# Kernel optimization log

Hardware: AMD Instinct MI355X
Metric: run time of the kernel (lower is better)

The kernel has to match this reference:

```python
import jax, jax.numpy as jnp
import numpy as np

EMBED_DIM = 2048
N_HEAD = 16
N_KV_HEAD = 4
HEAD_DIM = EMBED_DIM // N_HEAD  # 128
GROUP = N_HEAD // N_KV_HEAD     # 4
SCALE = HEAD_DIM ** -0.5
B, T = 2, 2048


def setup_inputs() -> dict:
    key = jax.random.key(0)
    ks = jax.random.split(key, 5)
    s = 0.02
    # weights stored as [in, out] (y = x @ W); equivalent to torch Linear W.T
    return {
        "x": jax.random.normal(ks[0], (B, T, EMBED_DIM), jnp.float32),
        "Wq": jax.random.normal(ks[1], (EMBED_DIM, EMBED_DIM), jnp.float32) * s,
        "Wk": jax.random.normal(ks[2], (EMBED_DIM, N_KV_HEAD * HEAD_DIM), jnp.float32) * s,
        "Wv": jax.random.normal(ks[3], (EMBED_DIM, N_KV_HEAD * HEAD_DIM), jnp.float32) * s,
        "Wo": jax.random.normal(ks[4], (EMBED_DIM, EMBED_DIM), jnp.float32) * s,
    }


def reference(x, Wq, Wk, Wv, Wo):
    # Prefill path (T>1, no cache): GQA causal attention, eval mode (dropout=0).
    Bq, Tq, C = x.shape
    q = (x @ Wq).reshape(Bq, Tq, N_HEAD, HEAD_DIM).transpose(0, 2, 1, 3)      # (B,Hq,T,D)
    k = (x @ Wk).reshape(Bq, Tq, N_KV_HEAD, HEAD_DIM).transpose(0, 2, 1, 3)  # (B,Hkv,T,D)
    v = (x @ Wv).reshape(Bq, Tq, N_KV_HEAD, HEAD_DIM).transpose(0, 2, 1, 3)
    # expand_kv: each kv head repeated GROUP times consecutively
    k = jnp.repeat(k, GROUP, axis=1)  # (B,Hq,T,D)
    v = jnp.repeat(v, GROUP, axis=1)
    scores = jnp.einsum("bhqd,bhkd->bhqk", q, k) * SCALE
    causal = jnp.tril(jnp.ones((Tq, Tq), dtype=bool))
    scores = jnp.where(causal[None, None], scores, jnp.finfo(scores.dtype).min)
    probs = jax.nn.softmax(scores, axis=-1)
    atten = jnp.einsum("bhqk,bhkd->bhqd", probs, v)
    atten = atten.transpose(0, 2, 1, 3).reshape(Bq, Tq, C)
    out = atten @ Wo
    return out
```

## Files before the change

### kernel.cpp

```cpp
#include <hip/hip_runtime.h>

typedef unsigned short u16;
typedef unsigned int   u32;
typedef __attribute__((ext_vector_type(4))) float  f32x4;
typedef __attribute__((ext_vector_type(8))) __bf16 bf16x8;

#define EMBED 2048
#define NH    16
#define NKV   4
#define HD    128
#define TT    2048
#define BB    2
#define MROWS (BB*TT)
#define QSCALE 0.08838834764831845f

#define QELEMS ((size_t)BB*NH*TT*HD)
#define KELEMS ((size_t)BB*NKV*TT*HD)

#define AS1(p) (__attribute__((address_space(1))) void*)(void*)(p)
#define AS3(p) (__attribute__((address_space(3))) void*)(void*)(p)


static __device__ __forceinline__ u16 f2b(float f){
  union { float f; u32 u; } v; v.f = f;
  u32 u = v.u;
  u32 r = u + 0x7FFFu + ((u >> 16) & 1u);
  return (u16)(r >> 16);
}

__global__ __launch_bounds__(256) void cvt_f32_bf16(const float* __restrict__ in,
                                                    u16* __restrict__ out, int n4){
  int i = blockIdx.x * 256 + threadIdx.x;
  if (i >= n4) return;
  float4 v = ((const float4*)in)[i];
  uint2 o;
  o.x = (u32)f2b(v.x) | ((u32)f2b(v.y) << 16);
  o.y = (u32)f2b(v.z) | ((u32)f2b(v.w) << 16);
  ((uint2*)out)[i] = o;
}

__global__ __launch_bounds__(256) void trans_w2(const float* __restrict__ in0, u16* __restrict__ out0,
                                                const float* __restrict__ in1, u16* __restrict__ out1,
                                                int R, int C){
  const float* in = blockIdx.z ? in1 : in0;
  u16*        out = blockIdx.z ? out1 : out0;
  __shared__ u16 tile[32][33];
  int c0 = blockIdx.x * 32, r0 = blockIdx.y * 32;
  int tx = threadIdx.x & 31, ty = threadIdx.x >> 5;
  #pragma unroll
  for (int j = 0; j < 32; j += 8)
    tile[ty + j][tx] = f2b(in[(size_t)(r0 + ty + j) * C + c0 + tx]);
  __syncthreads();
  #pragma unroll
  for (int j = 0; j < 32; j += 8)
    out[(size_t)(c0 + ty + j) * R + r0 + tx] = tile[tx][ty + j];
}

__global__ __launch_bounds__(256) void trans_v(const u16* __restrict__ in,
                                               u16* __restrict__ out){
  __shared__ u16 tile[32][33];
  int d0 = (blockIdx.x & 3) * 32;
  int t0 = ((blockIdx.x >> 2) & 63) * 32;
  int bh = blockIdx.x >> 8;
  const u16* ip = in  + (size_t)bh * TT * HD;
  u16*       op = out + (size_t)bh * TT * HD;
  int tx = threadIdx.x & 31, ty = threadIdx.x >> 5;
  #pragma unroll
  for (int j = 0; j < 32; j += 8)
    tile[ty + j][tx] = ip[(size_t)(t0 + ty + j) * HD + d0 + tx];
  __syncthreads();
  #pragma unroll
  for (int j = 0; j < 32; j += 8)
    op[(size_t)(d0 + ty + j) * TT + t0 + tx] = tile[tx][ty + j];
}

template<int EPI>
__global__ __launch_bounds__(256)
void gemm_bt(const u16* __restrict__ A, const u16* __restrict__ Bt,
             void* __restrict__ outp, int N, int K){
  __shared__ __align__(16) u16 As[2][128*32];
  __shared__ __align__(16) u16 Bs[2][128*32];
  int tid  = threadIdx.x;
  int lane = tid & 63, w = tid >> 6;
  int nwg = gridDim.x;
  int bid = blockIdx.x;
  bid = (bid & 7) * (nwg >> 3) + (bid >> 3);
  int nbn  = N >> 7;
  int brow = (bid / nbn) * 128;
  int bcol = (bid % nbn) * 128;

  auto stage = [&](int buf, int kt){
    #pragma unroll
    for (int j = 0; j < 2; ++j){
      int boff  = w * 2048 + j * 1024;
      int chunk = (boff >> 4) + lane;
      int row   = chunk >> 2;
      int cko   = chunk & 3;
      const u16* ga = A  + (size_t)(brow + row) * K + kt + cko * 8;
      const u16* gb = Bt + (size_t)(bcol + row) * K + kt + cko * 8;
      __builtin_amdgcn_global_load_lds(AS1(ga), AS3(&As[buf][boff >> 1]), 16, 0, 0);
      __builtin_amdgcn_global_load_lds(AS1(gb), AS3(&Bs[buf][boff >> 1]), 16, 0, 0);
    }
  };

  int lr = lane & 15, lg = lane >> 4, lk = lg * 8;
  int wr = (w >> 1) * 64, wc = (w & 1) * 64;

  f32x4 acc[4][4];
  #pragma unroll
  for (int m = 0; m < 4; ++m)
    #pragma unroll
    for (int n = 0; n < 4; ++n)
      #pragma unroll
      for (int r = 0; r < 4; ++r) acc[m][n][r] = 0.f;

  int NT = K >> 5;
  stage(0, 0);
  asm volatile("s_waitcnt vmcnt(0)" ::: "memory");
  __syncthreads();
  int cur = 0;
  for (int t = 0; t < NT; ++t){
    if (t + 1 < NT) stage(cur ^ 1, (t + 1) * 32);
    const u16* as = As[cur];
    const u16* bs = Bs[cur];
    bf16x8 af[4], bfv[4];
    #pragma unroll
    for (int m = 0; m < 4; ++m) af[m]  = *(const bf16x8*)(as + (wr + m*16 + lr)*32 + lk);
    #pragma unroll
    for (int n = 0; n < 4; ++n) bfv[n] = *(const bf16x8*)(bs + (wc + n*16 + lr)*32 + lk);
    #pragma unroll
    for (int m = 0; m < 4; ++m)
      #pragma unroll
      for (int n = 0; n < 4; ++n)
        acc[m][n] = __builtin_amdgcn_mfma_f32_16x16x32_bf16(af[m], bfv[n], acc[m][n], 0, 0, 0);
    asm volatile("s_waitcnt vmcnt(0)" ::: "memory");
    __syncthreads();
    cur ^= 1;
  }

  if (EPI == 0){
    float* o = (float*)outp;
    #pragma unroll
    for (int m = 0; m < 4; ++m)
      #pragma unroll
      for (int r = 0; r < 4; ++r){
        int rowg = brow + wr + m*16 + lg*4 + r;
        float* orow = o + (size_t)rowg * N + bcol + wc + lr;
        #pragma unroll
        for (int n = 0; n < 4; ++n) orow[n*16] = acc[m][n][r];
      }
  } else {
    u16* qb = (u16*)outp;
    u16* kb = qb + QELEMS;
    u16* vb = kb + KELEMS;
    int hb = bcol >> 7;
    int b  = brow >> 11;
    u16* hp; float s;
    if (hb < 16)      { hp = qb + ((size_t)(b*NH  +  hb     )) * TT * HD; s = QSCALE; }
    else if (hb < 20) { hp = kb + ((size_t)(b*NKV + (hb-16))) * TT * HD; s = 1.0f; }
    else              { hp = vb + ((size_t)(b*NKV + (hb-20))) * TT * HD; s = 1.0f; }
    #pragma unroll
    for (int m = 0; m < 4; ++m)
      #pragma unroll
      for (int r = 0; r < 4; ++r){
        int t = (brow + wr + m*16 + lg*4 + r) & (TT - 1);
        #pragma unroll
        for (int n = 0; n < 4; ++n){
          int d = wc + n*16 + lr;
          hp[(size_t)t * HD + d] = f2b(acc[m][n][r] * s);
        }
      }
  }
}

__global__ __launch_bounds__(256)
void attn_kernel(const u16* __restrict__ qb, const u16* __restrict__ kb,
                 const u16* __restrict__ vtb, u16* __restrict__ ob){
  __shared__ __align__(16) u16 Ks[2][64*128];
  __shared__ __align__(16) u16 Vs[2][128*64];
  int tid = threadIdx.x, lane = tid & 63, w = tid >> 6;
  int nwg = gridDim.x;
  int bid = blockIdx.x;
  bid = (bid & 7) * (nwg >> 3) + (bid >> 3);
  int pair = bid & 15;
  int h    = (bid >> 4) & 15;
  int b    = bid >> 8;
  int hkv  = h >> 2;
  int j  = lane & 15, g = lane >> 4, lk = g * 8;
  int gh = g >> 1;
  int sw = (j & 7) << 3;

  const u16* qbase = qb  + ((size_t)b * NH  + h  ) * TT * HD;
  const u16* kbase = kb  + ((size_t)b * NKV + hkv) * TT * HD;
  const u16* vbase = vtb + ((size_t)b * NKV + hkv) * HD * TT;

  auto stage = [&](int buf, int kt){
    #pragma unroll
    for (int i = 0; i < 4; ++i){
      int c  = i * 256 + tid;
      int ub = (i * 256 + w * 64) * 8;
      int kr = c >> 4, kc = (c & 15) ^ (kr & 7);
      const u16* gk = kbase + (size_t)(kt * 64 + kr) * HD + kc * 8;
      __builtin_amdgcn_global_load_lds(AS1(gk), AS3(&Ks[buf][ub]), 16, 0, 0);
      int vr = c >> 3, vc = (c & 7) ^ (vr & 7);
      const u16* gv = vbase + (size_t)vr * TT + kt * 64 + vc * 8;
      __builtin_amdgcn_global_load_lds(AS1(gv), AS3(&Vs[buf][ub]), 16, 0, 0);
    }
  };

  for (int half = 0; half < 2; ++half){
    int qt = half ? (31 - pair) : pair;
    int q0 = qt * 64 + w * 16;

    bf16x8 aq[4];
    #pragma unroll
    for (int s = 0; s < 4; ++s)
      aq[s] = *(const bf16x8*)(qbase + (size_t)(q0 + j) * HD + s*32 + lk);

    f32x4 o_acc[8];
    #pragma unroll
    for (int dt = 0; dt < 8; ++dt)
      #pragma unroll
      for (int r = 0; r < 4; ++r) o_acc[dt][r] = 0.f;
    float mrow = -1e30f, lrow = 0.f;

    __builtin_amdgcn_s_barrier();
    stage(0, 0);
    int cur = 0;
    for (int kt = 0; kt <= qt; ++kt){
      __builtin_amdgcn_s_barrier();
      if (kt < qt){
        stage(cur ^ 1, kt + 1);
        asm volatile("s_waitcnt vmcnt(8)" ::: "memory");
      } else {
        asm volatile("s_waitcnt vmcnt(0)" ::: "memory");
      }
      __builtin_amdgcn_s_barrier();

      const u16* ks = Ks[cur];
      f32x4 sc[4];
      #pragma unroll
      for (int c = 0; c < 4; ++c)
        #pragma unroll
        for (int r = 0; r < 4; ++r) sc[c][r] = 0.f;
      __builtin_amdgcn_s_setprio(1);
      #pragma unroll
      for (int c = 0; c < 4; ++c){
        const u16* kp = ks + (c*16 + j) * 128;
        #pragma unroll
        for (int s = 0; s < 4; ++s){
          bf16x8 kf = *(const bf16x8*)(kp + (((s*32) + lk) ^ sw));
          sc[c] = __builtin_amdgcn_mfma_f32_16x16x32_bf16(kf, aq[s], sc[c], 0, 0, 0);
        }
      }
      __builtin_amdgcn_s_setprio(0);
      if (kt == qt){
        int qg = q0 + j;
        #pragma unroll
        for (int c = 0; c < 4; ++c)
          #pragma unroll
          for (int r = 0; r < 4; ++r)
            if (kt*64 + c*16 + g*4 + r > qg) sc[c][r] = -1e30f;
      }
      float tm = fmaxf(fmaxf(fmaxf(sc[0][0], sc[0][1]), fmaxf(sc[0][2], sc[0][3])),
                       fmaxf(fmaxf(sc[1][0], sc[1][1]), fmaxf(sc[1][2], sc[1][3])));
      tm = fmaxf(tm, fmaxf(fmaxf(fmaxf(sc[2][0], sc[2][1]), fmaxf(sc[2][2], sc[2][3])),
                           fmaxf(fmaxf(sc[3][0], sc[3][1]), fmaxf(sc[3][2], sc[3][3]))));
      tm = fmaxf(tm, __shfl_xor(tm, 16));
      tm = fmaxf(tm, __shfl_xor(tm, 32));
      if (__any((tm > mrow + 8.f) ? 1 : 0)){
        float mnew  = fmaxf(mrow, tm);
        float alpha = __expf(mrow - mnew);
        mrow = mnew;
        lrow *= alpha;
        #pragma unroll
        for (int r = 0; r < 4; ++r){
          float ar = __shfl(alpha, (lane & 48) | (g*4 + r));
          #pragma unroll
          for (int dt = 0; dt < 8; ++dt) o_acc[dt][r] *= ar;
        }
      }
      float rs = 0.f;
      #pragma unroll
      for (int c = 0; c < 4; ++c)
        #pragma unroll
        for (int r = 0; r < 4; ++r){
          float p = __expf(sc[c][r] - mrow);
          sc[c][r] = p;
          rs += p;
        }
      rs += __shfl_xor(rs, 16);
      rs += __shfl_xor(rs, 32);
      lrow += rs;
      u32 pk[4][2];
      #pragma unroll
      for (int c = 0; c < 4; ++c){
        asm("v_cvt_pk_bf16_f32 %0, %1, %2" : "=v"(pk[c][0]) : "v"(sc[c][0]), "v"(sc[c][1]));
        asm("v_cvt_pk_bf16_f32 %0, %1, %2" : "=v"(pk[c][1]) : "v"(sc[c][2]), "v"(sc[c][3]));
      }
      bf16x8 pa[2];
      #pragma unroll
      for (int kk = 0; kk < 2; ++kk){
        u32 a0 = pk[2*kk + gh][0],       a1 = pk[2*kk + gh][1];
        u32 b0 = pk[2*kk + (gh ^ 1)][0], b1 = pk[2*kk + (gh ^ 1)][1];
        u32 v16_0 = (u32)__shfl_xor((int)a0, 16), v16_1 = (u32)__shfl_xor((int)a1, 16);
        u32 v32_0 = (u32)__shfl_xor((int)b0, 32), v32_1 = (u32)__shfl_xor((int)b1, 32);
        u32 v48_0 = (u32)__shfl_xor((int)b0, 48), v48_1 = (u32)__shfl_xor((int)b1, 48);
        union { u32 uw[4]; bf16x8 v; } u;
        u.uw[0] = (g==0) ? pk[2*kk][0]   : (g==1) ? v48_0 : (g==2) ? v32_0 : v16_0;
        u.uw[1] = (g==0) ? pk[2*kk][1]   : (g==1) ? v48_1 : (g==2) ? v32_1 : v16_1;
        u.uw[2] = (g==0) ? v16_0 : (g==1) ? v32_0 : (g==2) ? v48_0 : pk[2*kk+1][0];
        u.uw[3] = (g==0) ? v16_1 : (g==1) ? v32_1 : (g==2) ? v48_1 : pk[2*kk+1][1];
        pa[kk] = u.v;
      }
      const u16* vs = Vs[cur];
      __builtin_amdgcn_s_setprio(1);
      #pragma unroll
      for (int dt = 0; dt < 8; ++dt){
        const u16* vp = vs + (dt*16 + j) * 64;
        #pragma unroll
        for (int kk = 0; kk < 2; ++kk){
          bf16x8 vf = *(const bf16x8*)(vp + (((kk*32) + lk) ^ sw));
          o_acc[dt] = __builtin_amdgcn_mfma_f32_16x16x32_bf16(pa[kk], vf, o_acc[dt], 0, 0, 0);
        }
      }
      __builtin_amdgcn_s_setprio(0);
      cur ^= 1;
    }
    #pragma unroll
    for (int r = 0; r < 4; ++r){
      float ls  = __shfl(lrow, (lane & 48) | (g*4 + r));
      float inv = 1.0f / ls;
      int t = q0 + g*4 + r;
      size_t base = ((size_t)b * TT + t) * EMBED + h * HD;
      #pragma unroll
      for (int dt = 0; dt < 8; ++dt)
        ob[base + dt*16 + j] = f2b(o_acc[dt][r] * inv);
    }
  }
}

extern "C" void kernel_launch(void* const* d_in, const int* in_sizes, int n_in,
                              void* d_out, int out_size, void* d_ws, size_t ws_size,
                              hipStream_t stream){
  const float* x  = (const float*)d_in[0];
  const float* Wq = (const float*)d_in[1];
  const float* Wk = (const float*)d_in[2];
  const float* Wv = (const float*)d_in[3];
  const float* Wo = (const float*)d_in[4];

  char* ws = (char*)d_ws;
  size_t off = 0;
  auto alloc = [&](size_t bytes){ void* p = ws + off; off += (bytes + 255) & ~(size_t)255; return p; };
  u16* xb    = (u16*)alloc((size_t)MROWS * EMBED * 2);
  u16* Wqkvt = (u16*)alloc((size_t)3072 * EMBED * 2);
  u16* Wot   = (u16*)alloc((size_t)EMBED * EMBED * 2);
  u16* qkv   = (u16*)alloc((QELEMS + 2*KELEMS) * 2);
  u16* vtb   = (u16*)alloc(KELEMS * 2);
  u16* ob    = (u16*)alloc((size_t)MROWS * EMBED * 2);

  u16* qb = qkv;
  u16* kb = qb + QELEMS;
  u16* vb = kb + KELEMS;

  cvt_f32_bf16<<<(MROWS*EMBED/4 + 255)/256, 256, 0, stream>>>(x, xb, MROWS*EMBED/4);
  trans_w2<<<dim3(EMBED/32, EMBED/32, 2), 256, 0, stream>>>(Wq, Wqkvt, Wo, Wot, EMBED, EMBED);
  trans_w2<<<dim3(512/32,   EMBED/32, 2), 256, 0, stream>>>(Wk, Wqkvt + (size_t)2048*EMBED,
                                                            Wv, Wqkvt + (size_t)2560*EMBED, EMBED, 512);

  gemm_bt<2><<<(MROWS/128)*(3072/128), 256, 0, stream>>>(xb, Wqkvt, qkv, 3072, EMBED);
  trans_v<<<4*64*BB*NKV, 256, 0, stream>>>(vb, vtb);

  attn_kernel<<<BB*NH*16, 256, 0, stream>>>(qb, kb, vtb, ob);

  gemm_bt<0><<<(MROWS/128)*(EMBED/128), 256, 0, stream>>>(ob, Wot, d_out, EMBED, EMBED);
}
```

Baseline: 313.3 us.

## Use 128-row query tiles with two 16-row subtiles per wave in attention

The attention kernel now gives each workgroup a 128-row query tile, and each wave handles 32 query rows as two 16-row subtiles sharing every K/V fragment read from LDS. This halves the K/V staging traffic per query row and doubles the MFMA work per LDS read. The paired causal-balancing scheme (pair / 31-pair) is replaced by a longest-first ordering across 512 blocks, and launch bounds request two workgroups per SIMD. In exchange, register pressure roughly doubles (two sets of accumulators and Q fragments), which may force spills or lower occupancy, and the per-block causal work is now unbalanced.

```diff
diff --git a/kernel.cpp b/kernel.cpp
--- a/kernel.cpp
+++ b/kernel.cpp
@@ -173,19 +173,20 @@
   }
 }
 
-__global__ __launch_bounds__(256)
+__global__ __launch_bounds__(256, 2)
 void attn_kernel(const u16* __restrict__ qb, const u16* __restrict__ kb,
                  const u16* __restrict__ vtb, u16* __restrict__ ob){
   __shared__ __align__(16) u16 Ks[2][64*128];
   __shared__ __align__(16) u16 Vs[2][128*64];
   int tid = threadIdx.x, lane = tid & 63, w = tid >> 6;
-  int nwg = gridDim.x;
   int bid = blockIdx.x;
-  bid = (bid & 7) * (nwg >> 3) + (bid >> 3);
-  int pair = bid & 15;
-  int h    = (bid >> 4) & 15;
-  int b    = bid >> 8;
-  int hkv  = h >> 2;
+  int decoded = (bid & 7) * 64 + (bid >> 3);
+  int grp = decoded >> 6;
+  int i   = decoded & 63;
+  int qt  = 15 - (i & 15);
+  int h   = (grp & 3) * 4 + (i >> 4);
+  int b   = grp >> 2;
+  int hkv = h >> 2;
   int j  = lane & 15, g = lane >> 4, lk = g * 8;
   int gh = g >> 1;
   int sw = (j & 7) << 3;
@@ -196,9 +197,9 @@
 
   auto stage = [&](int buf, int kt){
     #pragma unroll
-    for (int i = 0; i < 4; ++i){
-      int c  = i * 256 + tid;
-      int ub = (i * 256 + w * 64) * 8;
+    for (int ii = 0; ii < 4; ++ii){
+      int c  = ii * 256 + tid;
+      int ub = (ii * 256 + w * 64) * 8;
       int kr = c >> 4, kc = (c & 15) ^ (kr & 7);
       const u16* gk = kbase + (size_t)(kt * 64 + kr) * HD + kc * 8;
       __builtin_amdgcn_global_load_lds(AS1(gk), AS3(&Ks[buf][ub]), 16, 0, 0);
@@ -208,76 +209,80 @@
     }
   };
 
-  for (int half = 0; half < 2; ++half){
-    int qt = half ? (31 - pair) : pair;
-    int q0 = qt * 64 + w * 16;
-
-    bf16x8 aq[4];
-    #pragma unroll
-    for (int s = 0; s < 4; ++s)
-      aq[s] = *(const bf16x8*)(qbase + (size_t)(q0 + j) * HD + s*32 + lk);
-
-    f32x4 o_acc[8];
-    #pragma unroll
-    for (int dt = 0; dt < 8; ++dt)
-      #pragma unroll
-      for (int r = 0; r < 4; ++r) o_acc[dt][r] = 0.f;
-    float mrow = -1e30f, lrow = 0.f;
-
+  int q0w = qt * 128 + w * 32;
+
+  bf16x8 aqA[4], aqB[4];
+  #pragma unroll
+  for (int s = 0; s < 4; ++s){
+    aqA[s] = *(const bf16x8*)(qbase + (size_t)(q0w + j)      * HD + s*32 + lk);
+    aqB[s] = *(const bf16x8*)(qbase + (size_t)(q0w + 16 + j) * HD + s*32 + lk);
+  }
+
+  f32x4 oA[8], oB[8];
+  #pragma unroll
+  for (int dt = 0; dt < 8; ++dt)
+    #pragma unroll
+    for (int r = 0; r < 4; ++r){ oA[dt][r] = 0.f; oB[dt][r] = 0.f; }
+  float mA = -1e30f, lA = 0.f, mB = -1e30f, lB = 0.f;
+
+  int nst = 2 * qt + 2;
+  stage(0, 0);
+  int cur = 0;
+  for (int kt = 0; kt < nst; ++kt){
     __builtin_amdgcn_s_barrier();
-    stage(0, 0);
-    int cur = 0;
-    for (int kt = 0; kt <= qt; ++kt){
-      __builtin_amdgcn_s_barrier();
-      if (kt < qt){
-        stage(cur ^ 1, kt + 1);
-        asm volatile("s_waitcnt vmcnt(8)" ::: "memory");
-      } else {
-        asm volatile("s_waitcnt vmcnt(0)" ::: "memory");
-      }
-      __builtin_amdgcn_s_barrier();
-
-      const u16* ks = Ks[cur];
-      f32x4 sc[4];
+    if (kt + 1 < nst){
+      stage(cur ^ 1, kt + 1);
+      asm volatile("s_waitcnt vmcnt(8)" ::: "memory");
+    } else {
+      asm volatile("s_waitcnt vmcnt(0)" ::: "memory");
+    }
+    __builtin_amdgcn_s_barrier();
+
+    const u16* ks = Ks[cur];
+    f32x4 scA[4], scB[4];
+    #pragma unroll
+    for (int c = 0; c < 4; ++c)
+      #pragma unroll
+      for (int r = 0; r < 4; ++r){ scA[c][r] = 0.f; scB[c][r] = 0.f; }
+    __builtin_amdgcn_s_setprio(1);
+    #pragma unroll
+    for (int c = 0; c < 4; ++c){
+      const u16* kp = ks + (c*16 + j) * 128;
+      #pragma unroll
+      for (int s = 0; s < 4; ++s){
+        bf16x8 kf = *(const bf16x8*)(kp + (((s*32) + lk) ^ sw));
+        scA[c] = __builtin_amdgcn_mfma_f32_16x16x32_bf16(kf, aqA[s], scA[c], 0, 0, 0);
+        scB[c] = __builtin_amdgcn_mfma_f32_16x16x32_bf16(kf, aqB[s], scB[c], 0, 0, 0);
+      }
+    }
+    __builtin_amdgcn_s_setprio(0);
+    if (kt*64 + 63 > q0w){
+      int qgA = q0w + j, qgB = q0w + 16 + j;
       #pragma unroll
       for (int c = 0; c < 4; ++c)
         #pragma unroll
-        for (int r = 0; r < 4; ++r) sc[c][r] = 0.f;
-      __builtin_amdgcn_s_setprio(1);
-      #pragma unroll
-      for (int c = 0; c < 4; ++c){
-        const u16* kp = ks + (c*16 + j) * 128;
-        #pragma unroll
-        for (int s = 0; s < 4; ++s){
-          bf16x8 kf = *(const bf16x8*)(kp + (((s*32) + lk) ^ sw));
-          sc[c] = __builtin_amdgcn_mfma_f32_16x16x32_bf16(kf, aq[s], sc[c], 0, 0, 0);
-        }
-      }
-      __builtin_amdgcn_s_setprio(0);
-      if (kt == qt){
-        int qg = q0 + j;
-        #pragma unroll
-        for (int c = 0; c < 4; ++c)
-          #pragma unroll
-          for (int r = 0; r < 4; ++r)
-            if (kt*64 + c*16 + g*4 + r > qg) sc[c][r] = -1e30f;
-      }
-      float tm = fmaxf(fmaxf(fmaxf(sc[0][0], sc[0][1]), fmaxf(sc[0][2], sc[0][3])),
-                       fmaxf(fmaxf(sc[1][0], sc[1][1]), fmaxf(sc[1][2], sc[1][3])));
-      tm = fmaxf(tm, fmaxf(fmaxf(fmaxf(sc[2][0], sc[2][1]), fmaxf(sc[2][2], sc[2][3])),
-                           fmaxf(fmaxf(sc[3][0], sc[3][1]), fmaxf(sc[3][2], sc[3][3]))));
+        for (int r = 0; r < 4; ++r){
+          int kv = kt*64 + c*16 + g*4 + r;
+          if (kv > qgA) scA[c][r] = -1e30f;
+          if (kv > qgB) scB[c][r] = -1e30f;
+        }
+    }
+    {
+      float tm = fmaxf(fmaxf(fmaxf(scA[0][0], scA[0][1]), fmaxf(scA[0][2], scA[0][3])),
+                       fmaxf(fmaxf(scA[1][0], scA[1][1]), fmaxf(scA[1][2], scA[1][3])));
+      tm = fmaxf(tm, fmaxf(fmaxf(fmaxf(scA[2][0], scA[2][1]), fmaxf(scA[2][2], scA[2][3])),
+                           fmaxf(fmaxf(scA[3][0], scA[3][1]), fmaxf(scA[3][2], scA[3][3]))));
       tm = fmaxf(tm, __shfl_xor(tm, 16));
       tm = fmaxf(tm, __shfl_xor(tm, 32));
-      if (__any((tm > mrow + 8.f) ? 1 : 0)){
-        float mnew  = fmaxf(mrow, tm);
-        float alpha = __expf(mrow - mnew);
-        mrow = mnew;
-        lrow *= alpha;
+      if (__any((tm > mA + 8.f) ? 1 : 0)){
+        float mnew  = fmaxf(mA, tm);
+        float alpha = __expf(mA - mnew);
+        mA = mnew; lA *= alpha;
         #pragma unroll
         for (int r = 0; r < 4; ++r){
           float ar = __shfl(alpha, (lane & 48) | (g*4 + r));
           #pragma unroll
-          for (int dt = 0; dt < 8; ++dt) o_acc[dt][r] *= ar;
+          for (int dt = 0; dt < 8; ++dt) oA[dt][r] *= ar;
         }
       }
       float rs = 0.f;
@@ -285,57 +290,108 @@
       for (int c = 0; c < 4; ++c)
         #pragma unroll
         for (int r = 0; r < 4; ++r){
-          float p = __expf(sc[c][r] - mrow);
-          sc[c][r] = p;
-          rs += p;
+          float p = __expf(scA[c][r] - mA);
+          scA[c][r] = p; rs += p;
         }
       rs += __shfl_xor(rs, 16);
       rs += __shfl_xor(rs, 32);
-      lrow += rs;
-      u32 pk[4][2];
-      #pragma unroll
-      for (int c = 0; c < 4; ++c){
-        asm("v_cvt_pk_bf16_f32 %0, %1, %2" : "=v"(pk[c][0]) : "v"(sc[c][0]), "v"(sc[c][1]));
-        asm("v_cvt_pk_bf16_f32 %0, %1, %2" : "=v"(pk[c][1]) : "v"(sc[c][2]), "v"(sc[c][3]));
-      }
-      bf16x8 pa[2];
-      #pragma unroll
-      for (int kk = 0; kk < 2; ++kk){
-        u32 a0 = pk[2*kk + gh][0],       a1 = pk[2*kk + gh][1];
-        u32 b0 = pk[2*kk + (gh ^ 1)][0], b1 = pk[2*kk + (gh ^ 1)][1];
+      lA += rs;
+    }
+    {
+      float tm = fmaxf(fmaxf(fmaxf(scB[0][0], scB[0][1]), fmaxf(scB[0][2], scB[0][3])),
+                       fmaxf(fmaxf(scB[1][0], scB[1][1]), fmaxf(scB[1][2], scB[1][3])));
+      tm = fmaxf(tm, fmaxf(fmaxf(fmaxf(scB[2][0], scB[2][1]), fmaxf(scB[2][2], scB[2][3])),
+                           fmaxf(fmaxf(scB[3][0], scB[3][1]), fmaxf(scB[3][2], scB[3][3]))));
+      tm = fmaxf(tm, __shfl_xor(tm, 16));
+      tm = fmaxf(tm, __shfl_xor(tm, 32));
+      if (__any((tm > mB + 8.f) ? 1 : 0)){
+        float mnew  = fmaxf(mB, tm);
+        float alpha = __expf(mB - mnew);
+        mB = mnew; lB *= alpha;
+        #pragma unroll
+        for (int r = 0; r < 4; ++r){
+          float ar = __shfl(alpha, (lane & 48) | (g*4 + r));
+          #pragma unroll
+          for (int dt = 0; dt < 8; ++dt) oB[dt][r] *= ar;
+        }
+      }
+      float rs = 0.f;
+      #pragma unroll
+      for (int c = 0; c < 4; ++c)
+        #pragma unroll
+        for (int r = 0; r < 4; ++r){
+          float p = __expf(scB[c][r] - mB);
+          scB[c][r] = p; rs += p;
+        }
+      rs += __shfl_xor(rs, 16);
+      rs += __shfl_xor(rs, 32);
+      lB += rs;
+    }
+    u32 pkA[4][2], pkB[4][2];
+    #pragma unroll
+    for (int c = 0; c < 4; ++c){
+      asm("v_cvt_pk_bf16_f32 %0, %1, %2" : "=v"(pkA[c][0]) : "v"(scA[c][0]), "v"(scA[c][1]));
+      asm("v_cvt_pk_bf16_f32 %0, %1, %2" : "=v"(pkA[c][1]) : "v"(scA[c][2]), "v"(scA[c][3]));
+      asm("v_cvt_pk_bf16_f32 %0, %1, %2" : "=v"(pkB[c][0]) : "v"(scB[c][0]), "v"(scB[c][1]));
+      asm("v_cvt_pk_bf16_f32 %0, %1, %2" : "=v"(pkB[c][1]) : "v"(scB[c][2]), "v"(scB[c][3]));
+    }
+    bf16x8 paA[2], paB[2];
+    #pragma unroll
+    for (int kk = 0; kk < 2; ++kk){
+      {
+        u32 a0 = pkA[2*kk + gh][0],       a1 = pkA[2*kk + gh][1];
+        u32 b0 = pkA[2*kk + (gh ^ 1)][0], b1 = pkA[2*kk + (gh ^ 1)][1];
         u32 v16_0 = (u32)__shfl_xor((int)a0, 16), v16_1 = (u32)__shfl_xor((int)a1, 16);
         u32 v32_0 = (u32)__shfl_xor((int)b0, 32), v32_1 = (u32)__shfl_xor((int)b1, 32);
         u32 v48_0 = (u32)__shfl_xor((int)b0, 48), v48_1 = (u32)__shfl_xor((int)b1, 48);
         union { u32 uw[4]; bf16x8 v; } u;
-        u.uw[0] = (g==0) ? pk[2*kk][0]   : (g==1) ? v48_0 : (g==2) ? v32_0 : v16_0;
-        u.uw[1] = (g==0) ? pk[2*kk][1]   : (g==1) ? v48_1 : (g==2) ? v32_1 : v16_1;
-        u.uw[2] = (g==0) ? v16_0 : (g==1) ? v32_0 : (g==2) ? v48_0 : pk[2*kk+1][0];
-        u.uw[3] = (g==0) ? v16_1 : (g==1) ? v32_1 : (g==2) ? v48_1 : pk[2*kk+1][1];
-        pa[kk] = u.v;
-      }
-      const u16* vs = Vs[cur];
-      __builtin_amdgcn_s_setprio(1);
-      #pragma unroll
-      for (int dt = 0; dt < 8; ++dt){
-        const u16* vp = vs + (dt*16 + j) * 64;
-        #pragma unroll
-        for (int kk = 0; kk < 2; ++kk){
-          bf16x8 vf = *(const bf16x8*)(vp + (((kk*32) + lk) ^ sw));
-          o_acc[dt] = __builtin_amdgcn_mfma_f32_16x16x32_bf16(pa[kk], vf, o_acc[dt], 0, 0, 0);
-        }
-      }
-      __builtin_amdgcn_s_setprio(0);
-      cur ^= 1;
-    }
-    #pragma unroll
-    for (int r = 0; r < 4; ++r){
-      float ls  = __shfl(lrow, (lane & 48) | (g*4 + r));
-      float inv = 1.0f / ls;
-      int t = q0 + g*4 + r;
-      size_t base = ((size_t)b * TT + t) * EMBED + h * HD;
-      #pragma unroll
-      for (int dt = 0; dt < 8; ++dt)
-        ob[base + dt*16 + j] = f2b(o_acc[dt][r] * inv);
+        u.uw[0] = (g==0) ? pkA[2*kk][0]   : (g==1) ? v48_0 : (g==2) ? v32_0 : v16_0;
+        u.uw[1] = (g==0) ? pkA[2*kk][1]   : (g==1) ? v48_1 : (g==2) ? v32_1 : v16_1;
+        u.uw[2] = (g==0) ? v16_0 : (g==1) ? v32_0 : (g==2) ? v48_0 : pkA[2*kk+1][0];
+        u.uw[3] = (g==0) ? v16_1 : (g==1) ? v32_1 : (g==2) ? v48_1 : pkA[2*kk+1][1];
+        paA[kk] = u.v;
+      }
+      {
+        u32 a0 = pkB[2*kk + gh][0],       a1 = pkB[2*kk + gh][1];
+        u32 b0 = pkB[2*kk + (gh ^ 1)][0], b1 = pkB[2*kk + (gh ^ 1)][1];
+        u32 v16_0 = (u32)__shfl_xor((int)a0, 16), v16_1 = (u32)__shfl_xor((int)a1, 16);
+        u32 v32_0 = (u32)__shfl_xor((int)b0, 32), v32_1 = (u32)__shfl_xor((int)b1, 32);
+        u32 v48_0 = (u32)__shfl_xor((int)b0, 48), v48_1 = (u32)__shfl_xor((int)b1, 48);
+        union { u32 uw[4]; bf16x8 v; } u;
+        u.uw[0] = (g==0) ? pkB[2*kk][0]   : (g==1) ? v48_0 : (g==2) ? v32_0 : v16_0;
+        u.uw[1] = (g==0) ? pkB[2*kk][1]   : (g==1) ? v48_1 : (g==2) ? v32_1 : v16_1;
+        u.uw[2] = (g==0) ? v16_0 : (g==1) ? v32_0 : (g==2) ? v48_0 : pkB[2*kk+1][0];
+        u.uw[3] = (g==0) ? v16_1 : (g==1) ? v32_1 : (g==2) ? v48_1 : pkB[2*kk+1][1];
+        paB[kk] = u.v;
+      }
+    }
+    const u16* vs = Vs[cur];
+    __builtin_amdgcn_s_setprio(1);
+    #pragma unroll
+    for (int dt = 0; dt < 8; ++dt){
+      const u16* vp = vs + (dt*16 + j) * 64;
+      #pragma unroll
+      for (int kk = 0; kk < 2; ++kk){
+        bf16x8 vf = *(const bf16x8*)(vp + (((kk*32) + lk) ^ sw));
+        oA[dt] = __builtin_amdgcn_mfma_f32_16x16x32_bf16(paA[kk], vf, oA[dt], 0, 0, 0);
+        oB[dt] = __builtin_amdgcn_mfma_f32_16x16x32_bf16(paB[kk], vf, oB[dt], 0, 0, 0);
+      }
+    }
+    __builtin_amdgcn_s_setprio(0);
+    cur ^= 1;
+  }
+  #pragma unroll
+  for (int r = 0; r < 4; ++r){
+    float lsA = __shfl(lA, (lane & 48) | (g*4 + r));
+    float lsB = __shfl(lB, (lane & 48) | (g*4 + r));
+    float invA = 1.0f / lsA, invB = 1.0f / lsB;
+    int tA = q0w + g*4 + r, tB = tA + 16;
+    size_t baseA = ((size_t)b * TT + tA) * EMBED + h * HD;
+    size_t baseB = ((size_t)b * TT + tB) * EMBED + h * HD;
+    #pragma unroll
+    for (int dt = 0; dt < 8; ++dt){
+      ob[baseA + dt*16 + j] = f2b(oA[dt][r] * invA);
+      ob[baseB + dt*16 + j] = f2b(oB[dt][r] * invB);
     }
   }
 }
```

Result: slower. 356.7 us (+13.8%).
